# Optimization experiments

Hardware: AMD Instinct MI355X
Metric: run time of the kernel (lower is better)

The kernel has to match this reference:

```python
import jax, jax.numpy as jnp
import numpy as np
import math

SCALES = (128.0, 256.0, 512.0)
ASPECT_RATIOS = (0.5, 1.0, 2.0)
NUM_ANCHORS = len(SCALES) * len(ASPECT_RATIOS)  # 9
NMS_THRESHOLD = 0.7
PRENMS_TOPK = 6000
POST_TOPK = 300
MIN_SIZE = 16.0
DWH_CLAMP = math.log(1000.0 / 16)


def conv2d(x, w, b, pad):
    y = jax.lax.conv_general_dilated(
        x, w, window_strides=(1, 1), padding=[(pad, pad), (pad, pad)],
        dimension_numbers=('NCHW', 'OIHW', 'NCHW'))
    return y + b[None, :, None, None]


def generate_anchors(image_h, image_w, grid_h, grid_w, dtype):
    stride_h = image_h // grid_h
    stride_w = image_w // grid_w
    scales = jnp.asarray(SCALES, dtype)
    ar = jnp.asarray(ASPECT_RATIOS, dtype)
    h_r = jnp.sqrt(ar)
    w_r = 1.0 / h_r
    ws = (w_r[:, None] * scales[None, :]).reshape(-1)
    hs = (h_r[:, None] * scales[None, :]).reshape(-1)
    base = jnp.round(jnp.stack([-ws, -hs, ws, hs], axis=1) / 2)  # [A,4]
    sx = jnp.arange(grid_w, dtype=dtype) * stride_w
    sy = jnp.arange(grid_h, dtype=dtype) * stride_h
    yy, xx = jnp.meshgrid(sy, sx, indexing='ij')
    xx = xx.reshape(-1)
    yy = yy.reshape(-1)
    shifts = jnp.stack([xx, yy, xx, yy], axis=1)  # [gh*gw,4]
    anchors = (shifts[:, None, :] + base[None, :, :]).reshape(-1, 4)
    return anchors


def decode(deltas, anchors):
    # deltas, anchors: [N,4] -> pred boxes [N,4]
    w = anchors[:, 2] - anchors[:, 0]
    h = anchors[:, 3] - anchors[:, 1]
    cx = anchors[:, 0] + 0.5 * w
    cy = anchors[:, 1] + 0.5 * h
    dx, dy = deltas[:, 0], deltas[:, 1]
    dw = jnp.minimum(deltas[:, 2], DWH_CLAMP)
    dh = jnp.minimum(deltas[:, 3], DWH_CLAMP)
    pcx = dx * w + cx
    pcy = dy * h + cy
    pw = jnp.exp(dw) * w
    ph = jnp.exp(dh) * h
    return jnp.stack([pcx - 0.5 * pw, pcy - 0.5 * ph, pcx + 0.5 * pw, pcy + 0.5 * ph], axis=1)


def nms_keep(boxes, keep_init, thr):
    # boxes sorted by descending score; greedy NMS without NxN matrix.
    n = boxes.shape[0]
    area = (boxes[:, 2] - boxes[:, 0]) * (boxes[:, 3] - boxes[:, 1])
    idxs = jnp.arange(n)

    def body(i, keep):
        b = boxes[i]
        xl = jnp.maximum(b[0], boxes[:, 0])
        yt = jnp.maximum(b[1], boxes[:, 1])
        xr = jnp.minimum(b[2], boxes[:, 2])
        yb = jnp.minimum(b[3], boxes[:, 3])
        inter = jnp.clip(xr - xl, 0.0) * jnp.clip(yb - yt, 0.0)
        iou = inter / (area[i] + area - inter)
        sup = (iou > thr) & (idxs > i) & keep[i]
        return keep & ~sup

    return jax.lax.fori_loop(0, n, body, keep_init)


def setup_inputs() -> dict:
    key = jax.random.key(0)
    ks = jax.random.split(key, 4)
    C = 256
    feat = jax.random.normal(ks[0], (1, C, 160, 160), jnp.float32)
    image = jnp.zeros((1, 3, 2560, 2560), jnp.float32)  # only shape is used
    conv_w = 0.01 * jax.random.normal(ks[1], (C, C, 3, 3), jnp.float32)
    conv_b = jnp.zeros((C,), jnp.float32)
    cls_w = 0.01 * jax.random.normal(ks[2], (NUM_ANCHORS, C, 1, 1), jnp.float32)
    cls_b = jnp.zeros((NUM_ANCHORS,), jnp.float32)
    bbox_w = 0.01 * jax.random.normal(ks[3], (NUM_ANCHORS * 4, C, 1, 1), jnp.float32)
    bbox_b = jnp.zeros((NUM_ANCHORS * 4,), jnp.float32)
    return {'feat': feat, 'image': image, 'conv_w': conv_w, 'conv_b': conv_b,
            'cls_w': cls_w, 'cls_b': cls_b, 'bbox_w': bbox_w, 'bbox_b': bbox_b}


def reference(feat, image, conv_w, conv_b, cls_w, cls_b, bbox_w, bbox_b):
    gh, gw = feat.shape[-2:]
    ih, iw = image.shape[-2:]
    rpn_feat = jax.nn.relu(conv2d(feat, conv_w, conv_b, 1))
    cls = conv2d(rpn_feat, cls_w, cls_b, 0)     # [1,A,gh,gw]
    reg = conv2d(rpn_feat, bbox_w, bbox_b, 0)   # [1,4A,gh,gw]
    # match anchor order (h, w, anchor)
    scores = jnp.transpose(cls, (0, 2, 3, 1)).reshape(-1)
    deltas = jnp.transpose(reg.reshape(1, NUM_ANCHORS, 4, gh, gw), (0, 3, 4, 1, 2)).reshape(-1, 4)
    anchors = generate_anchors(ih, iw, gh, gw, feat.dtype)
    proposals = decode(deltas, anchors)
    scores = jax.nn.sigmoid(scores)
    # 1. pre-NMS top-k (top_k returns sorted descending)
    top_scores, idx = jax.lax.top_k(scores, PRENMS_TOPK)
    boxes = proposals[idx]
    # 2. clamp to image
    x1 = jnp.clip(boxes[:, 0], 0.0, iw)
    y1 = jnp.clip(boxes[:, 1], 0.0, ih)
    x2 = jnp.clip(boxes[:, 2], 0.0, iw)
    y2 = jnp.clip(boxes[:, 3], 0.0, ih)
    boxes = jnp.stack([x1, y1, x2, y2], axis=1)
    # 3. remove small boxes (as invalid for NMS)
    valid = ((x2 - x1) >= MIN_SIZE) & ((y2 - y1) >= MIN_SIZE)
    # 4. greedy NMS
    keep = nms_keep(boxes, valid, NMS_THRESHOLD)
    # 5. post-NMS top-k; suppressed entries padded with score -1
    final_scores = jnp.where(keep, top_scores, -1.0)
    fs, fidx = jax.lax.top_k(final_scores, POST_TOPK)
    return jnp.concatenate([boxes[fidx], fs[:, None]], axis=1)  # [POST_TOPK, 5]
```

## Files before the change

### kernel.cpp

```cpp
#include <hip/hip_runtime.h>
#include <math.h>

typedef unsigned long long u64;
typedef unsigned int u32;

#define HH 160
#define WW 160
#define CC 256
#define NPX 25600
#define NA 9
#define NSC 230400
#define K_SEL 6000
#define SEL_PAD 6016
#define IMS 2560.0f
#define DWH 4.135166556742356f

struct SelState { u64 prefix; u32 r; u32 cnt; };

#define OFF_BOXES   0u
#define OFF_SCORES  3686400u
#define OFF_KEYS    4608000u
#define OFF_STATE   7499776u
#define OFF_SELK    7500032u
#define OFF_SX1     7548160u
#define OFF_SY1     7572224u
#define OFF_SX2     7596288u
#define OFF_SY2     7620352u
#define OFF_SSC     7644416u
#define OFF_MASKR   11503104u
#define OFF_WT      16028160u
#define OFF_HIST    18387456u
#define OFF_RPN     27869184u

__constant__ float c_bx1[9] = {-91.f,-181.f,-362.f,-64.f,-128.f,-256.f,-45.f,-91.f,-181.f};
__constant__ float c_by1[9] = {-45.f,-91.f,-181.f,-64.f,-128.f,-256.f,-91.f,-181.f,-362.f};
__constant__ float c_bx2[9] = { 91.f, 181.f, 362.f, 64.f, 128.f, 256.f, 45.f, 91.f, 181.f};
__constant__ float c_by2[9] = { 45.f,  91.f, 181.f, 64.f, 128.f, 256.f, 91.f, 181.f, 362.f};

__device__ inline u64 shfl64(u64 v, int src) {
  int lo = (int)(v & 0xFFFFFFFFull), hi = (int)(v >> 32);
  lo = __shfl(lo, src, 64); hi = __shfl(hi, src, 64);
  return ((u64)(u32)hi << 32) | (u32)lo;
}
__device__ inline u64 shfl64_up(u64 v, int delta) {
  int lo = __shfl_up((int)(v & 0xFFFFFFFFull), delta, 64);
  int hi = __shfl_up((int)(v >> 32), delta, 64);
  return ((u64)(u32)hi << 32) | (u32)lo;
}
__device__ inline u64 shfl64_xor(u64 v, int mask) {
  int lo = __shfl_xor((int)(v & 0xFFFFFFFFull), mask, 64);
  int hi = __shfl_xor((int)(v >> 32), mask, 64);
  return ((u64)(u32)hi << 32) | (u32)lo;
}

__global__ __launch_bounds__(256) void wtrz_k(const float* __restrict__ w, float* __restrict__ wT,
                                              u32* __restrict__ hist, SelState* st) {
  int b = blockIdx.x;
  int tid = threadIdx.x;
  if (b < 144) {
    __shared__ float t[64][65];
    int kb = b % 36;
    int ob = b / 36;
    for (int it = 0; it < 16; it++) {
      int idx = it * 256 + tid;
      int row = idx >> 6, colk = idx & 63;
      t[row][colk] = w[(size_t)(ob * 64 + row) * 2304 + kb * 64 + colk];
    }
    __syncthreads();
    for (int it = 0; it < 16; it++) {
      int idx = it * 256 + tid;
      int krow = idx >> 6, occ = idx & 63;
      wT[(size_t)(kb * 64 + krow) * 256 + ob * 64 + occ] = t[occ][krow];
    }
  } else {
    int zb = (b - 144) * 1024 + tid * 4;
    *(uint4*)&hist[zb] = make_uint4(0, 0, 0, 0);
    if (b == 144 && tid == 0) { st->prefix = 0; st->r = K_SEL; st->cnt = 0; }
  }
}

__global__ __launch_bounds__(256) void conv_k(const float* __restrict__ feat,
                                              const float* __restrict__ wT,
                                              const float* __restrict__ bias,
                                              float* __restrict__ outp) {
  int bx = blockIdx.x;
  int ct = bx % 5;
  int rt = (bx / 5) % 40;
  int ot = bx / 200;
  int x0 = ct * 32, y0 = rt * 4, oc0 = ot * 64;

  __shared__ float ps[2][8][6][36];

  int tid = threadIdx.x;
  int lane = tid & 63;
  int wvu = __builtin_amdgcn_readfirstlane(tid >> 6);
  int col = lane & 31;
  int s = lane >> 5;
  int ocw = oc0 + wvu * 16;

  int s_off[7]; int s_lof[7]; bool s_val[7];
#pragma unroll
  for (int it = 0; it < 7; it++) {
    int idx = tid + it * 256;
    bool ex = (idx < 1632);
    int icl = idx / 204, rem = idx % 204;
    int r = rem / 34, c = rem % 34;
    int gy = y0 + r - 1, gx = x0 + c - 1;
    s_val[it] = ex && ((unsigned)gy < 160u) && ((unsigned)gx < 160u);
    s_off[it] = icl * NPX + gy * WW + gx;
    s_lof[it] = ex ? ((icl * 6 + r) * 36 + c) : 0;
    if (!ex) s_lof[it] = -1;
  }

  float acc0[16], acc1[16];
#pragma unroll
  for (int i = 0; i < 16; i++) { acc0[i] = 0.f; acc1[i] = 0.f; }

  float st[7];
#pragma unroll
  for (int it = 0; it < 7; it++) {
    float v = 0.f;
    if (s_val[it]) v = feat[s_off[it]];
    if (s_lof[it] >= 0) (&ps[0][0][0][0])[s_lof[it]] = v;
  }
  __syncthreads();

  for (int c8 = 0; c8 < 32; c8++) {
    if (c8 < 31) {
      int icn = (c8 + 1) * 8;
#pragma unroll
      for (int it = 0; it < 7; it++) {
        st[it] = 0.f;
        if (s_val[it]) st[it] = feat[icn * NPX + s_off[it]];
      }
    }
    int buf = c8 & 1;
    int ic0 = c8 * 8;
    for (int icl = 0; icl < 8; icl++) {
      float p[4][3];
#pragma unroll
      for (int rr = 0; rr < 4; rr++)
#pragma unroll
        for (int cc = 0; cc < 3; cc++)
          p[rr][cc] = ps[buf][icl][2 * s + rr][col + cc];
      const float* wb = wT + (size_t)(ic0 + icl) * 9 * 256 + ocw;
#pragma unroll
      for (int dy = 0; dy < 3; dy++) {
#pragma unroll
        for (int dx = 0; dx < 3; dx++) {
          const float* wr = wb + (dy * 3 + dx) * 256;
#pragma unroll
          for (int i = 0; i < 16; i++) {
            float wv_ = wr[i];
            acc0[i] += wv_ * p[dy][dx];
            acc1[i] += wv_ * p[dy + 1][dx];
          }
        }
      }
    }
    if (c8 < 31) {
      __syncthreads();
      float* dst = &ps[buf ^ 1][0][0][0];
#pragma unroll
      for (int it = 0; it < 7; it++)
        if (s_lof[it] >= 0) dst[s_lof[it]] = st[it];
      __syncthreads();
    }
  }
#pragma unroll
  for (int i = 0; i < 16; i++) {
    int oc = ocw + i;
    float bv = bias[oc];
    size_t base = (size_t)oc * NPX + (y0 + 2 * s) * WW + x0 + col;
    outp[base] = fmaxf(acc0[i] + bv, 0.f);
    outp[base + WW] = fmaxf(acc1[i] + bv, 0.f);
  }
}

__global__ __launch_bounds__(256) void heads_k(const float* __restrict__ rpn,
                                               const float* __restrict__ cls_w,
                                               const float* __restrict__ cls_b,
                                               const float* __restrict__ bbox_w,
                                               const float* __restrict__ bbox_b,
                                               float4* __restrict__ boxes,
                                               float* __restrict__ scores,
                                               u64* __restrict__ keys) {
  __shared__ float sf[32][260];
  __shared__ float so[45][33];
  int tid = threadIdx.x;
  int px0 = blockIdx.x * 32;
  for (int idx = tid; idx < 8192; idx += 256) {
    int c = idx >> 5, p = idx & 31;
    sf[p][c] = rpn[(size_t)c * NPX + px0 + p];
  }
  __syncthreads();
  int p = tid & 31, g = tid >> 5;
  for (int oi = 0; oi < 6; oi++) {
    int o = g + oi * 8;
    if (o >= 45) break;
    const float* wr = (o < 9) ? (cls_w + o * CC) : (bbox_w + (o - 9) * CC);
    float bsum = (o < 9) ? cls_b[o] : bbox_b[o - 9];
    float s = 0.f;
    for (int c = 0; c < CC; c += 4) {
      float4 f = *(const float4*)&sf[p][c];
      float4 wv = *(const float4*)&wr[c];
      s += f.x * wv.x; s += f.y * wv.y; s += f.z * wv.z; s += f.w * wv.w;
    }
    so[o][p] = s + bsum;
  }
  __syncthreads();
  for (int t = tid; t < 288; t += 256) {
    int a = t >> 5, pp = t & 31;
    int px = px0 + pp;
    int y = px / 160, x = px - y * 160;
    float logit = so[a][pp];
    float sc = 1.f / (1.f + expf(-logit));
    float ddx = so[9 + 4 * a][pp], ddy = so[10 + 4 * a][pp];
    float ddw = fminf(so[11 + 4 * a][pp], DWH);
    float ddh = fminf(so[12 + 4 * a][pp], DWH);
    float ax1 = x * 16.f + c_bx1[a];
    float ay1 = y * 16.f + c_by1[a];
    float ax2 = x * 16.f + c_bx2[a];
    float ay2 = y * 16.f + c_by2[a];
    float aw = ax2 - ax1, ah = ay2 - ay1;
    float cx = ax1 + 0.5f * aw, cy = ay1 + 0.5f * ah;
    float pcx = ddx * aw + cx, pcy = ddy * ah + cy;
    float pw = expf(ddw) * aw, phh = expf(ddh) * ah;
    float x1 = pcx - 0.5f * pw, y1 = pcy - 0.5f * phh;
    float x2 = pcx + 0.5f * pw, y2 = pcy + 0.5f * phh;
    x1 = fminf(fmaxf(x1, 0.f), IMS); x2 = fminf(fmaxf(x2, 0.f), IMS);
    y1 = fminf(fmaxf(y1, 0.f), IMS); y2 = fminf(fmaxf(y2, 0.f), IMS);
    int gidx = px * 9 + a;
    boxes[gidx] = make_float4(x1, y1, x2, y2);
    scores[gidx] = sc;
    u32 sb = __float_as_uint(sc);
    u32 mono = (sb & 0x80000000u) ? ~sb : (sb | 0x80000000u);
    keys[gidx] = ((u64)mono << 32) | (u64)(0xFFFFFFFFu - (u32)gidx);
  }
}

__global__ __launch_bounds__(256) void hist_k(const u64* __restrict__ keys,
                                              const SelState* __restrict__ st,
                                              u32* __restrict__ hist,
                                              int wbits, int bitsdone) {
  int idx = blockIdx.x * 256 + threadIdx.x;
  int lane = threadIdx.x & 63;
  u64 k = keys[idx];
  int shift = 64 - bitsdone - wbits;
  bool active = true;
  if (bitsdone > 0) active = ((k >> (64 - bitsdone)) == st->prefix);
  u32 digit = (u32)((k >> shift) & (u64)((1 << wbits) - 1));
  u64 act = __ballot(active);
  u64 todo = act;
  while (todo) {
    int src = __builtin_ctzll(todo);
    u32 d0 = (u32)__shfl((int)digit, src, 64);
    u64 m = __ballot(digit == d0) & act;
    if (lane == src) atomicAdd(&hist[d0], (u32)__popcll(m & todo));
    todo &= ~m;
  }
}

__global__ __launch_bounds__(1024) void scan_k(const u32* __restrict__ hist,
                                               SelState* st, int wbits) {
  __shared__ u32 tsum[1024];
  __shared__ u32 wsum[16];
  int tid = threadIdx.x;
  int lane = tid & 63, wv = tid >> 6;
  int nbins = 1 << wbits;
  int bpt = nbins >> 10;
  u32 r = st->r;
  u32 s = 0;
  for (int b = 0; b < bpt; b++) s += hist[tid * bpt + b];
  tsum[tid] = s;
  u32 v = s;
#pragma unroll
  for (int off = 1; off < 64; off <<= 1) v += (u32)__shfl_xor((int)v, off, 64);
  if (lane == 0) wsum[wv] = v;
  __syncthreads();
  if (tid == 0) {
    u32 cum = 0;
    int ws = 15;
    while (ws > 0 && cum + wsum[ws] < r) { cum += wsum[ws]; ws--; }
    int t = ws * 64 + 63, tend = ws * 64;
    while (t > tend && cum + tsum[t] < r) { cum += tsum[t]; t--; }
    int b = t * bpt + bpt - 1, bend = t * bpt;
    while (b > bend && cum + hist[b] < r) { cum += hist[b]; b--; }
    st->prefix = (st->prefix << wbits) | (u64)(u32)b;
    st->r = r - cum;
  }
}

__global__ __launch_bounds__(256) void compact_k(const u64* __restrict__ keys,
                                                 SelState* st, u64* __restrict__ selk) {
  __shared__ u32 wbase[4];
  __shared__ u32 blkbase;
  int tid = threadIdx.x;
  int lane = tid & 63, wv = tid >> 6;
  int idx = blockIdx.x * 256 + tid;
  u64 k = keys[idx];
  bool sel = (k >= st->prefix);
  u64 m = __ballot(sel);
  u32 wcnt = (u32)__popcll(m);
  u32 before = (u32)__popcll(m & ((1ull << lane) - 1ull));
  if (lane == 0) wbase[wv] = wcnt;
  __syncthreads();
  if (tid == 0) {
    u32 b0 = wbase[0], b1 = wbase[1], b2 = wbase[2], b3 = wbase[3];
    u32 tot = b0 + b1 + b2 + b3;
    blkbase = tot ? atomicAdd(&st->cnt, tot) : 0u;
    wbase[0] = 0; wbase[1] = b0; wbase[2] = b0 + b1; wbase[3] = b0 + b1 + b2;
  }
  __syncthreads();
  if (sel) selk[blkbase + wbase[wv] + before] = k;
}

__global__ __launch_bounds__(64) void rank_k(const u64* __restrict__ selk,
                                             const float4* __restrict__ boxes,
                                             const float* __restrict__ scores,
                                             float* sx1, float* sy1, float* sx2, float* sy2, float* ssc) {
  __shared__ __align__(16) u64 sk[SEL_PAD];
  int lane = threadIdx.x;
  for (int i = lane; i < SEL_PAD; i += 64) sk[i] = (i < K_SEL) ? selk[i] : 0ull;
  __syncthreads();
  int n = blockIdx.x * 64 + lane;
  u64 myk = (n < K_SEL) ? selk[n] : ~0ull;
  int cnt = 0;
  const ulonglong2* sk2 = (const ulonglong2*)sk;
#pragma unroll 8
  for (int j = 0; j < SEL_PAD / 2; j++) {
    ulonglong2 kk = sk2[j];
    cnt += (kk.x > myk) ? 1 : 0;
    cnt += (kk.y > myk) ? 1 : 0;
  }
  if (n < K_SEL) {
    u32 oidx = 0xFFFFFFFFu - (u32)(myk & 0xFFFFFFFFull);
    float4 b = boxes[oidx];
    sx1[cnt] = b.x; sy1[cnt] = b.y; sx2[cnt] = b.z; sy2[cnt] = b.w;
    ssc[cnt] = scores[oidx];
  }
}

__global__ __launch_bounds__(256) void mask_k(const float* __restrict__ sx1, const float* __restrict__ sy1,
                                              const float* __restrict__ sx2, const float* __restrict__ sy2,
                                              u64* __restrict__ maskR) {
  __shared__ float jb[5][3008];
  int tid = threadIdx.x;
  int wv = tid >> 6, lane = tid & 63;
  int ibase = blockIdx.x * 32 + wv * 8;
  float ix1[8], iy1[8], ix2[8], iy2[8], ia[8];
#pragma unroll
  for (int r = 0; r < 8; r++) {
    int i = ibase + r;
    ix1[r] = sx1[i]; iy1[r] = sy1[i]; ix2[r] = sx2[i]; iy2[r] = sy2[i];
    ia[r] = (ix2[r] - ix1[r]) * (iy2[r] - iy1[r]);
  }
  for (int half = 0; half < 2; half++) {
    int j0 = half * 3008;
    __syncthreads();
    for (int idx = tid; idx < 3008; idx += 256) {
      int j = j0 + idx;
      bool v = j < K_SEL;
      float a = v ? sx1[j] : 0.f;
      float b = v ? sy1[j] : 0.f;
      float c = v ? sx2[j] : 0.f;
      float d = v ? sy2[j] : 0.f;
      jb[0][idx] = a; jb[1][idx] = b; jb[2][idx] = c; jb[3][idx] = d;
      jb[4][idx] = (c - a) * (d - b);
    }
    __syncthreads();
    for (int wi = 0; wi < 47; wi++) {
      int w = half * 47 + wi;
      int jl = wi * 64 + lane;
      int j = j0 + jl;
      float jx1 = jb[0][jl], jy1 = jb[1][jl], jx2 = jb[2][jl], jy2 = jb[3][jl], ja = jb[4][jl];
      bool jv = j < K_SEL;
#pragma unroll
      for (int r = 0; r < 8; r++) {
        int i = ibase + r;
        float xl = fmaxf(ix1[r], jx1), yt = fmaxf(iy1[r], jy1);
        float xr = fminf(ix2[r], jx2), yb = fminf(iy2[r], jy2);
        float iw = fmaxf(xr - xl, 0.f), ihh = fmaxf(yb - yt, 0.f);
        float inter = iw * ihh;
        bool sup = jv && (j > i) && (inter > 0.7f * (ia[r] + ja - inter));
        u64 bits = __ballot(sup);
        if (lane == 0 && i < K_SEL) maskR[(size_t)i * 94 + w] = bits;
      }
    }
  }
}

__global__ __launch_bounds__(1024) void nmsf_k(const u64* __restrict__ maskR,
                                               const float* __restrict__ sx1, const float* __restrict__ sy1,
                                               const float* __restrict__ sx2, const float* __restrict__ sy2,
                                               const float* __restrict__ ssc, float* __restrict__ out) {
  __shared__ u64 tile[6016];
  __shared__ u64 skept[96];
  __shared__ u64 svalid[94];
  __shared__ u32 dead32[188];
  __shared__ u32 pre[95];
  int tid = threadIdx.x;
  int wv = tid >> 6, lane = tid & 63;

  if (tid < 96) skept[tid] = 0ull;
  if (tid < 188) dead32[tid] = 0u;
  for (int w = wv; w < 94; w += 16) {
    int p = w * 64 + lane;
    float bw = sx2[p] - sx1[p], bh = sy2[p] - sy1[p];
    bool ok = (p < K_SEL) && (bw >= 16.f) && (bh >= 16.f);
    u64 bits = __ballot(ok);
    if (lane == 0) svalid[w] = bits;
  }
  u64 stg[6];
#pragma unroll
  for (int j = 0; j < 6; j++) {
    int i = tid + j * 1024;
    stg[j] = (i < 6016) ? maskR[i] : 0ull;
  }
#pragma unroll
  for (int j = 0; j < 6; j++) {
    int i = tid + j * 1024;
    if (i < 6016) tile[i] = stg[j];
  }
  __syncthreads();

  for (int c = 0; c < 94; c++) {
    if (c < 93) {
      const u64* tb = maskR + (size_t)(c + 1) * 6016;
#pragma unroll
      for (int j = 0; j < 6; j++) {
        int i = tid + j * 1024;
        stg[j] = (i < 6016) ? tb[i] : 0ull;
      }
    }
    if (wv == 0) {
      u64 deadc = ((u64)dead32[2 * c + 1] << 32) | (u64)dead32[2 * c];
      u64 cur = svalid[c] & ~deadc;
      u64 d = tile[lane * 94 + c];
      u64 kept = 0;
      while (cur) {
        u64 inc = ((cur >> lane) & 1ull) ? d : 0ull;
#pragma unroll
        for (int off = 1; off < 64; off <<= 1) {
          u64 t = shfl64_up(inc, off);
          if (lane >= off) inc |= t;
        }
        u64 ex = shfl64_up(inc, 1);
        if (lane == 0) ex = 0ull;
        bool in_cur = (cur >> lane) & 1ull;
        bool suppd = (ex >> lane) & 1ull;
        u64 safe = __ballot(in_cur && !suppd);
        u64 y = ((safe >> lane) & 1ull) ? d : 0ull;
#pragma unroll
        for (int off = 1; off < 64; off <<= 1) y |= shfl64_xor(y, off);
        kept |= safe;
        cur &= ~safe;
        cur &= ~y;
      }
      if (lane == 0) skept[c] = kept;
    }
    __syncthreads();
    u64 km = skept[c];
    if (km) {
      for (int idx = tid; idx < 94 * 16; idx += 1024) {
        int w = idx % 94, g = idx / 94;
        u64 acc = 0;
#pragma unroll
        for (int q = 0; q < 4; q++) {
          int l = g * 4 + q;
          if ((km >> l) & 1ull) acc |= tile[l * 94 + w];
        }
        if (acc) {
          u32 alo = (u32)acc, ahi = (u32)(acc >> 32);
          if (alo) atomicOr(&dead32[2 * w], alo);
          if (ahi) atomicOr(&dead32[2 * w + 1], ahi);
        }
      }
    }
    __syncthreads();
    if (c < 93) {
#pragma unroll
      for (int j = 0; j < 6; j++) {
        int i = tid + j * 1024;
        if (i < 6016) tile[i] = stg[j];
      }
      __syncthreads();
    }
  }

  if (tid == 0) {
    u32 s = 0;
    for (int w = 0; w < 94; w++) { pre[w] = s; s += (u32)__popcll(skept[w]); }
    pre[94] = s;
  }
  __syncthreads();
  u32 total = pre[94];
  for (int p = tid; p < K_SEL; p += 1024) {
    int w = p >> 6, b = p & 63;
    u64 word = skept[w];
    u32 kb = pre[w] + (u32)__popcll(word & ((1ull << b) - 1ull));
    bool kept = (word >> b) & 1ull;
    int slot = -1; float sc = -1.f;
    if (kept) {
      if (kb < 300) { slot = (int)kb; sc = ssc[p]; }
    } else {
      u32 s2 = total + (u32)p - kb;
      if (s2 < 300) slot = (int)s2;
    }
    if (slot >= 0) {
      out[slot * 5 + 0] = sx1[p];
      out[slot * 5 + 1] = sy1[p];
      out[slot * 5 + 2] = sx2[p];
      out[slot * 5 + 3] = sy2[p];
      out[slot * 5 + 4] = sc;
    }
  }
}

extern "C" void kernel_launch(void* const* d_in, const int* in_sizes, int n_in,
                              void* d_out, int out_size, void* d_ws, size_t ws_size,
                              hipStream_t stream) {
  const float* feat   = (const float*)d_in[0];
  const float* conv_w = (const float*)d_in[2];
  const float* conv_b = (const float*)d_in[3];
  const float* cls_w  = (const float*)d_in[4];
  const float* cls_b  = (const float*)d_in[5];
  const float* bbox_w = (const float*)d_in[6];
  const float* bbox_b = (const float*)d_in[7];
  float* out = (float*)d_out;
  char* ws = (char*)d_ws;

  float*  rpn    = (float*)(ws + OFF_RPN);
  float4* boxes  = (float4*)(ws + OFF_BOXES);
  float*  scores = (float*)(ws + OFF_SCORES);
  u64*    keys   = (u64*)(ws + OFF_KEYS);
  SelState* st   = (SelState*)(ws + OFF_STATE);
  u64*    selk   = (u64*)(ws + OFF_SELK);
  float*  sx1    = (float*)(ws + OFF_SX1);
  float*  sy1    = (float*)(ws + OFF_SY1);
  float*  sx2    = (float*)(ws + OFF_SX2);
  float*  sy2    = (float*)(ws + OFF_SY2);
  float*  ssc    = (float*)(ws + OFF_SSC);
  u64*    maskR  = (u64*)(ws + OFF_MASKR);
  float*  wT     = (float*)(ws + OFF_WT);
  u32*    hist   = (u32*)(ws + OFF_HIST);

  wtrz_k<<<184, 256, 0, stream>>>(conv_w, wT, hist, st);
  conv_k<<<800, 256, 0, stream>>>(feat, wT, conv_b, rpn);
  heads_k<<<800, 256, 0, stream>>>(rpn, cls_w, cls_b, bbox_w, bbox_b, boxes, scores, keys);

  hist_k<<<900, 256, 0, stream>>>(keys, st, hist,         13,  0);
  scan_k<<<1, 1024, 0, stream>>>(hist,         st, 13);
  hist_k<<<900, 256, 0, stream>>>(keys, st, hist +  8192, 13, 13);
  scan_k<<<1, 1024, 0, stream>>>(hist +  8192, st, 13);
  hist_k<<<900, 256, 0, stream>>>(keys, st, hist + 16384, 13, 26);
  scan_k<<<1, 1024, 0, stream>>>(hist + 16384, st, 13);
  hist_k<<<900, 256, 0, stream>>>(keys, st, hist + 24576, 13, 39);
  scan_k<<<1, 1024, 0, stream>>>(hist + 24576, st, 13);
  hist_k<<<900, 256, 0, stream>>>(keys, st, hist + 32768, 12, 52);
  scan_k<<<1, 1024, 0, stream>>>(hist + 32768, st, 12);

  compact_k<<<900, 256, 0, stream>>>(keys, st, selk);
  rank_k<<<94, 64, 0, stream>>>(selk, boxes, scores, sx1, sy1, sx2, sy2, ssc);
  mask_k<<<188, 256, 0, stream>>>(sx1, sy1, sx2, sy2, maskR);
  nmsf_k<<<1, 1024, 0, stream>>>(maskR, sx1, sy1, sx2, sy2, ssc, out);
}
```

Before: 1.133 ms.

## Double-buffer NMS mask tiles and cut radix-select passes to four

The single-block NMS kernel now double-buffers its shared-memory mask tile. Waves 1-15 store the prefetched next tile while wave 0 runs the serial per-chunk scan, and the following tile is loaded from global memory after the barrier. This removes one barrier per chunk and hides the global load latency behind compute. Separately, the radix top-k select goes from five 13/12-bit passes to a 13-bit pass plus three 17-bit passes, dropping one hist/scan launch pair. The cost is much larger histograms, which need a larger zeroing grid in wtrz_k and longer single-block scans.

```diff
diff --git a/kernel.cpp b/kernel.cpp
--- a/kernel.cpp
+++ b/kernel.cpp
@@ -394,13 +394,14 @@
                                                const float* __restrict__ sx1, const float* __restrict__ sy1,
                                                const float* __restrict__ sx2, const float* __restrict__ sy2,
                                                const float* __restrict__ ssc, float* __restrict__ out) {
-  __shared__ u64 tile[6016];
+  __shared__ u64 tile[2][6016];
   __shared__ u64 skept[96];
   __shared__ u64 svalid[94];
   __shared__ u32 dead32[188];
   __shared__ u32 pre[95];
   int tid = threadIdx.x;
   int wv = tid >> 6, lane = tid & 63;
+  int sbase = tid - 64;
 
   if (tid < 96) skept[tid] = 0ull;
   if (tid < 188) dead32[tid] = 0u;
@@ -411,32 +412,27 @@
     u64 bits = __ballot(ok);
     if (lane == 0) svalid[w] = bits;
   }
-  u64 stg[6];
-#pragma unroll
-  for (int j = 0; j < 6; j++) {
-    int i = tid + j * 1024;
-    stg[j] = (i < 6016) ? maskR[i] : 0ull;
-  }
-#pragma unroll
-  for (int j = 0; j < 6; j++) {
-    int i = tid + j * 1024;
-    if (i < 6016) tile[i] = stg[j];
-  }
-  __syncthreads();
-
+  u64 stg[7];
+  if (tid >= 64) {
+#pragma unroll
+    for (int j = 0; j < 7; j++) {
+      int i = sbase + j * 960;
+      if (i < 6016) tile[0][i] = maskR[i];
+    }
+#pragma unroll
+    for (int j = 0; j < 7; j++) {
+      int i = sbase + j * 960;
+      stg[j] = (i < 6016) ? maskR[6016 + i] : 0ull;
+    }
+  }
+  __syncthreads();
+
+  int buf = 0;
   for (int c = 0; c < 94; c++) {
-    if (c < 93) {
-      const u64* tb = maskR + (size_t)(c + 1) * 6016;
-#pragma unroll
-      for (int j = 0; j < 6; j++) {
-        int i = tid + j * 1024;
-        stg[j] = (i < 6016) ? tb[i] : 0ull;
-      }
-    }
     if (wv == 0) {
       u64 deadc = ((u64)dead32[2 * c + 1] << 32) | (u64)dead32[2 * c];
       u64 cur = svalid[c] & ~deadc;
-      u64 d = tile[lane * 94 + c];
+      u64 d = tile[buf][lane * 94 + c];
       u64 kept = 0;
       while (cur) {
         u64 inc = ((cur >> lane) & 1ull) ? d : 0ull;
@@ -458,8 +454,22 @@
         cur &= ~y;
       }
       if (lane == 0) skept[c] = kept;
+    } else if (c < 93) {
+#pragma unroll
+      for (int j = 0; j < 7; j++) {
+        int i = sbase + j * 960;
+        if (i < 6016) tile[buf ^ 1][i] = stg[j];
+      }
     }
     __syncthreads();
+    if (c < 92 && tid >= 64) {
+      const u64* tb = maskR + (size_t)(c + 2) * 6016;
+#pragma unroll
+      for (int j = 0; j < 7; j++) {
+        int i = sbase + j * 960;
+        stg[j] = (i < 6016) ? tb[i] : 0ull;
+      }
+    }
     u64 km = skept[c];
     if (km) {
       for (int idx = tid; idx < 94 * 16; idx += 1024) {
@@ -468,7 +478,7 @@
 #pragma unroll
         for (int q = 0; q < 4; q++) {
           int l = g * 4 + q;
-          if ((km >> l) & 1ull) acc |= tile[l * 94 + w];
+          if ((km >> l) & 1ull) acc |= tile[buf][l * 94 + w];
         }
         if (acc) {
           u32 alo = (u32)acc, ahi = (u32)(acc >> 32);
@@ -478,14 +488,7 @@
       }
     }
     __syncthreads();
-    if (c < 93) {
-#pragma unroll
-      for (int j = 0; j < 6; j++) {
-        int i = tid + j * 1024;
-        if (i < 6016) tile[i] = stg[j];
-      }
-      __syncthreads();
-    }
+    buf ^= 1;
   }
 
   if (tid == 0) {
@@ -545,20 +548,23 @@
   float*  wT     = (float*)(ws + OFF_WT);
   u32*    hist   = (u32*)(ws + OFF_HIST);
 
-  wtrz_k<<<184, 256, 0, stream>>>(conv_w, wT, hist, st);
+  u32* h0 = hist;
+  u32* h1 = hist + 8192;
+  u32* h2 = hist + 139264;
+  u32* h3 = hist + 270336;
+
+  wtrz_k<<<536, 256, 0, stream>>>(conv_w, wT, hist, st);
   conv_k<<<800, 256, 0, stream>>>(feat, wT, conv_b, rpn);
   heads_k<<<800, 256, 0, stream>>>(rpn, cls_w, cls_b, bbox_w, bbox_b, boxes, scores, keys);
 
-  hist_k<<<900, 256, 0, stream>>>(keys, st, hist,         13,  0);
-  scan_k<<<1, 1024, 0, stream>>>(hist,         st, 13);
-  hist_k<<<900, 256, 0, stream>>>(keys, st, hist +  8192, 13, 13);
-  scan_k<<<1, 1024, 0, stream>>>(hist +  8192, st, 13);
-  hist_k<<<900, 256, 0, stream>>>(keys, st, hist + 16384, 13, 26);
-  scan_k<<<1, 1024, 0, stream>>>(hist + 16384, st, 13);
-  hist_k<<<900, 256, 0, stream>>>(keys, st, hist + 24576, 13, 39);
-  scan_k<<<1, 1024, 0, stream>>>(hist + 24576, st, 13);
-  hist_k<<<900, 256, 0, stream>>>(keys, st, hist + 32768, 12, 52);
-  scan_k<<<1, 1024, 0, stream>>>(hist + 32768, st, 12);
+  hist_k<<<900, 256, 0, stream>>>(keys, st, h0, 13,  0);
+  scan_k<<<1, 1024, 0, stream>>>(h0, st, 13);
+  hist_k<<<900, 256, 0, stream>>>(keys, st, h1, 17, 13);
+  scan_k<<<1, 1024, 0, stream>>>(h1, st, 17);
+  hist_k<<<900, 256, 0, stream>>>(keys, st, h2, 17, 30);
+  scan_k<<<1, 1024, 0, stream>>>(h2, st, 17);
+  hist_k<<<900, 256, 0, stream>>>(keys, st, h3, 17, 47);
+  scan_k<<<1, 1024, 0, stream>>>(h3, st, 17);
 
   compact_k<<<900, 256, 0, stream>>>(keys, st, selk);
   rank_k<<<94, 64, 0, stream>>>(selk, boxes, scores, sx1, sy1, sx2, sy2, ssc);
```

New measurement: 1.227 ms. 1.08x slower.
